# Performance work log

Measured on AMD Instinct MI355X. Metric: run time of the kernel, lower is better.

## Reference

```python
import jax, jax.numpy as jnp
import numpy as np

N, IN_DIM, OUT_DIM, NUM_EXPERTS, TOP_K = 8192, 1024, 1024, 8, 2


def setup_inputs() -> dict:
    key = jax.random.key(0)
    ks = jax.random.split(key, 5)
    s_in = 1.0 / np.sqrt(IN_DIM)
    x = jax.random.normal(ks[0], (N, IN_DIM), dtype=jnp.float32)
    # per-expert Linear weights: [E, in, out] (torch Linear weight is [out,in]; we store transposed)
    W = jax.random.uniform(ks[1], (NUM_EXPERTS, IN_DIM, OUT_DIM), jnp.float32, -s_in, s_in)
    b = jax.random.uniform(ks[2], (NUM_EXPERTS, OUT_DIM), jnp.float32, -s_in, s_in)
    Wg = jax.random.uniform(ks[3], (IN_DIM, NUM_EXPERTS), jnp.float32, -s_in, s_in)
    bg = jax.random.uniform(ks[4], (NUM_EXPERTS,), jnp.float32, -s_in, s_in)
    return {"x": x, "W": W, "b": b, "Wg": Wg, "bg": bg}


def reference(x, W, b, Wg, bg):
    # gating scores [N, E]
    scores = x @ Wg + bg
    # top-k mask
    _, top_idx = jax.lax.top_k(scores, TOP_K)  # [N, k]
    mask = jnp.zeros_like(scores).at[jnp.arange(x.shape[0])[:, None], top_idx].set(1.0)
    masked = jnp.where(mask == 0, -jnp.inf, scores)
    gating_weights = jax.nn.softmax(masked, axis=-1)  # [N, E]
    # all-expert linear: [N, E, out]
    expert_outputs = jnp.einsum('ni,eio->neo', x, W) + b
    # weighted combine over experts
    return jnp.einsum('ne,neo->no', gating_weights, expert_outputs)
```

## Files before the change

kernel.cpp:

```cpp
#include <hip/hip_runtime.h>

#define N_TOK 8192
#define IN_DIM 1024
#define OUT_DIM 1024
#define NE 8
#define TILE_SH 12288

typedef short short8 __attribute__((ext_vector_type(8)));
typedef float f32x4 __attribute__((ext_vector_type(4)));
typedef ushort ushort4v __attribute__((ext_vector_type(4)));

__device__ __forceinline__ ushort f2bf(float f) {
    union { float f; unsigned u; } v; v.f = f;
    unsigned u = v.u;
    unsigned r = (u + 0x7fffu + ((u >> 16) & 1u)) >> 16;
    return (ushort)r;
}

__device__ __forceinline__ float bf2f(short s) {
    union { unsigned u; float f; } v;
    v.u = ((unsigned)(unsigned short)s) << 16;
    return v.f;
}

__device__ __forceinline__ void gl_lds16(const short* g, short* l) {
    __builtin_amdgcn_global_load_lds(
        (const __attribute__((address_space(1))) unsigned int*)g,
        (__attribute__((address_space(3))) unsigned int*)l, 16, 0, 0);
}

__global__ __launch_bounds__(256) void prep(const float* __restrict__ x,
                                            const float* __restrict__ Wg,
                                            const float* __restrict__ bg,
                                            const float* __restrict__ W,
                                            short* __restrict__ xb,
                                            short* __restrict__ wt,
                                            unsigned* __restrict__ choice,
                                            float2* __restrict__ wts) {
    __shared__ ushort tile[32][33];
    int bid = blockIdx.x;
    int t = threadIdx.x;
    if (bid < 512) {
        int wid = t >> 6, lane = t & 63;
        int tok0 = bid * 16 + wid * 4;
        float acc[4][8];
        #pragma unroll
        for (int tk = 0; tk < 4; ++tk)
            #pragma unroll
            for (int e = 0; e < 8; ++e) acc[tk][e] = 0.f;

        #pragma unroll
        for (int it = 0; it < 4; ++it) {
            int j = it * 256 + lane * 4;
            float4 wa[4], wb[4];
            #pragma unroll
            for (int r = 0; r < 4; ++r) {
                wa[r] = *(const float4*)(Wg + (size_t)(j + r) * 8);
                wb[r] = *(const float4*)(Wg + (size_t)(j + r) * 8 + 4);
            }
            #pragma unroll
            for (int tk = 0; tk < 4; ++tk) {
                const float* xr = x + (size_t)(tok0 + tk) * IN_DIM;
                float4 v = *(const float4*)(xr + j);
                ushort4v o;
                o[0] = f2bf(v.x); o[1] = f2bf(v.y); o[2] = f2bf(v.z); o[3] = f2bf(v.w);
                *(ushort4v*)(xb + (size_t)(tok0 + tk) * IN_DIM + j) = o;
                #pragma unroll
                for (int r = 0; r < 4; ++r) {
                    float xv = (r == 0) ? v.x : (r == 1) ? v.y : (r == 2) ? v.z : v.w;
                    acc[tk][0] += xv * wa[r].x; acc[tk][1] += xv * wa[r].y;
                    acc[tk][2] += xv * wa[r].z; acc[tk][3] += xv * wa[r].w;
                    acc[tk][4] += xv * wb[r].x; acc[tk][5] += xv * wb[r].y;
                    acc[tk][6] += xv * wb[r].z; acc[tk][7] += xv * wb[r].w;
                }
            }
        }
        #pragma unroll
        for (int tk = 0; tk < 4; ++tk)
            #pragma unroll
            for (int e = 0; e < 8; ++e)
                #pragma unroll
                for (int off = 32; off; off >>= 1)
                    acc[tk][e] += __shfl_xor(acc[tk][e], off, 64);
        if (lane == 0) {
            #pragma unroll
            for (int tk = 0; tk < 4; ++tk) {
                float s[8];
                #pragma unroll
                for (int e = 0; e < 8; ++e) s[e] = acc[tk][e] + bg[e];
                int i0 = 0;
                #pragma unroll
                for (int e = 1; e < 8; ++e) if (s[e] > s[i0]) i0 = e;
                int i1 = (i0 == 0) ? 1 : 0;
                #pragma unroll
                for (int e = 0; e < 8; ++e) if (e != i0 && s[e] > s[i1]) i1 = e;
                float e0 = 1.f, e1 = __expf(s[i1] - s[i0]);
                float inv = 1.f / (e0 + e1);
                choice[tok0 + tk] = (unsigned)i0 | ((unsigned)i1 << 8);
                wts[tok0 + tk] = make_float2(e0 * inv, e1 * inv);
            }
        }
    } else {
        int id = bid - 512;
        int nt = id & 31, kt = (id >> 5) & 31, e = id >> 10;
        int r = t >> 3;
        int c4 = (t & 7) * 4;
        const float4 v = *(const float4*)(W + (((size_t)e * 1024 + kt * 32 + r) * 1024) + nt * 32 + c4);
        tile[c4 + 0][r] = f2bf(v.x);
        tile[c4 + 1][r] = f2bf(v.y);
        tile[c4 + 2][r] = f2bf(v.z);
        tile[c4 + 3][r] = f2bf(v.w);
        __syncthreads();
        int n = t >> 3, kq = (t & 7) * 4;
        ushort4v o;
        o[0] = tile[n][kq + 0]; o[1] = tile[n][kq + 1];
        o[2] = tile[n][kq + 2]; o[3] = tile[n][kq + 3];
        *(ushort4v*)(wt + (((size_t)e * 1024 + nt * 32 + n) * 1024) + kt * 32 + kq) = o;
    }
}

__global__ __launch_bounds__(1024) void bucket(const unsigned* __restrict__ choice,
                                               int* __restrict__ counts,
                                               int* __restrict__ entries,
                                               int* __restrict__ inv0,
                                               int* __restrict__ inv1) {
    int e = blockIdx.x;
    int t = threadIdx.x;
    int wid = t >> 6, lane = t & 63;
    __shared__ int wsum[16];
    unsigned c[8];
    #pragma unroll
    for (int chunk = 0; chunk < 8; ++chunk) c[chunk] = choice[chunk * 1024 + t];
    int base = 0;
    #pragma unroll
    for (int chunk = 0; chunk < 8; ++chunk) {
        int tok = chunk * 1024 + t;
        int which = ((int)(c[chunk] & 255u) == e) ? 0
                  : (((int)((c[chunk] >> 8) & 255u) == e) ? 1 : -1);
        unsigned long long m = __ballot(which >= 0);
        if (lane == 0) wsum[wid] = __popcll(m);
        __syncthreads();
        int woff = base;
        #pragma unroll
        for (int i = 0; i < 16; ++i) if (i < wid) woff += wsum[i];
        int tot = 0;
        #pragma unroll
        for (int i = 0; i < 16; ++i) tot += wsum[i];
        if (which >= 0) {
            int rank = __popcll(m & ((1ull << lane) - 1ull));
            int idx = woff + rank;
            entries[e * N_TOK + idx] = tok;
            if (which == 0) inv0[tok] = idx; else inv1[tok] = idx;
        }
        base += tot;
        __syncthreads();
    }
    if (t == 0) counts[e] = base;
}

__global__ __launch_bounds__(256, 2) void moe_gemm(const short* __restrict__ xb,
                                                   const short* __restrict__ wt,
                                                   const float* __restrict__ bias,
                                                   const int* __restrict__ counts,
                                                   const int* __restrict__ entries,
                                                   short* __restrict__ ys) {
    int lin = blockIdx.x;
    int e = lin & 7;
    int inner = lin >> 3;
    int ct = inner & 3, rt = inner >> 2;
    int cnt = counts[e];
    if (rt * 128 >= cnt) return;
    int rows = min(128, cnt - rt * 128);
    int base_e = 0;
    #pragma unroll
    for (int i = 0; i < NE; ++i) base_e += (i < e) ? counts[i] : 0;

    __shared__ __align__(16) short lds[3 * TILE_SH];
    __shared__ int tok_sh[128];

    int t = threadIdx.x, wid = t >> 6, lane = t & 63;
    int ebase = e * N_TOK + rt * 128;
    if (t < 128) tok_sh[t] = (t < rows) ? entries[ebase + t] : entries[ebase];
    __syncthreads();

    int chunkoff = (((t & 3) ^ ((t >> 2) & 3)) * 8);
    const short* asrc0 = xb + (size_t)tok_sh[t >> 2] * IN_DIM + chunkoff;
    const short* asrc1 = xb + (size_t)tok_sh[64 + (t >> 2)] * IN_DIM + chunkoff;
    const short* bsrc0 = wt + ((size_t)e * OUT_DIM + ct * 256 + (t >> 2)) * IN_DIM + chunkoff;
    const short* bsrc1 = bsrc0 + (size_t)64 * IN_DIM;
    const short* bsrc2 = bsrc0 + (size_t)128 * IN_DIM;
    const short* bsrc3 = bsrc0 + (size_t)192 * IN_DIM;
    int dst8 = t * 8;

    int wr = wid >> 1, wc = wid & 1;
    int frow = lane & 15, fslot = lane >> 4;
    int rslot = (fslot ^ (frow & 3)) * 8;
    int aoff[4], boff[8];
    #pragma unroll
    for (int mi = 0; mi < 4; ++mi) aoff[mi] = (wr * 64 + mi * 16 + frow) * 32 + rslot;
    #pragma unroll
    for (int ni = 0; ni < 8; ++ni) boff[ni] = (wc * 128 + ni * 16 + frow) * 32 + rslot;

    f32x4 acc[4][8];
    #pragma unroll
    for (int mi = 0; mi < 4; ++mi)
        #pragma unroll
        for (int ni = 0; ni < 8; ++ni) acc[mi][ni] = (f32x4)(0.0f);

    short8 caf[4], cbf[8];

#define STAGE(BUF, KT)                                                        \
    {                                                                         \
        short* nb = lds + (BUF) * TILE_SH;                                    \
        int nk = (KT) * 32;                                                   \
        gl_lds16(asrc0 + nk, nb + dst8);                                      \
        gl_lds16(asrc1 + nk, nb + 2048 + dst8);                               \
        gl_lds16(bsrc0 + nk, nb + 4096 + dst8);                               \
        gl_lds16(bsrc1 + nk, nb + 6144 + dst8);                               \
        gl_lds16(bsrc2 + nk, nb + 8192 + dst8);                               \
        gl_lds16(bsrc3 + nk, nb + 10240 + dst8);                              \
    }

#define LOADFRAGS(BUF)                                                        \
    {                                                                         \
        const short* Ab = lds + (BUF) * TILE_SH;                              \
        const short* Bb = Ab + 4096;                                          \
        _Pragma("unroll")                                                     \
        for (int mi = 0; mi < 4; ++mi) caf[mi] = *(const short8*)(Ab + aoff[mi]); \
        _Pragma("unroll")                                                     \
        for (int ni = 0; ni < 8; ++ni) cbf[ni] = *(const short8*)(Bb + boff[ni]); \
    }

#define GITER(NXTBUF, STGBUF, KTN, VN, DO_STAGE, DO_TAIL)                     \
    {                                                                         \
        if (DO_STAGE) STAGE(STGBUF, KTN);                                     \
        _Pragma("unroll")                                                     \
        for (int mi = 0; mi < 4; ++mi)                                        \
            _Pragma("unroll")                                                 \
            for (int ni = 0; ni < 8; ++ni)                                    \
                acc[mi][ni] = __builtin_amdgcn_mfma_f32_16x16x32_bf16(        \
                    caf[mi], cbf[ni], acc[mi][ni], 0, 0, 0);                  \
        asm volatile("s_waitcnt vmcnt(" VN ")" ::: "memory");                 \
        __builtin_amdgcn_s_barrier();                                         \
        __builtin_amdgcn_sched_barrier(0);   \
        if (DO_TAIL) LOADFRAGS(NXTBUF);                                       \
    }

    STAGE(0, 0);
    STAGE(1, 1);
    asm volatile("s_waitcnt vmcnt(6)" ::: "memory");
    __builtin_amdgcn_s_barrier();
    __builtin_amdgcn_sched_barrier(0);
    LOADFRAGS(0);

    for (int kt = 0; kt < 30; kt += 3) {
        GITER(1, 2, kt + 2, "6", 1, 1);
        GITER(2, 0, kt + 3, "6", 1, 1);
        GITER(0, 1, kt + 4, "6", 1, 1);
    }
    GITER(1, 0, 0, "0", 0, 1);
    GITER(0, 0, 0, "0", 0, 0);

#undef GITER
#undef LOADFRAGS
#undef STAGE

    __syncthreads();
    short* ep = lds;
    const float* be = bias + (size_t)e * OUT_DIM;
    #pragma unroll
    for (int ni = 0; ni < 8; ++ni) {
        int col = wc * 128 + ni * 16 + frow;
        float bv = be[ct * 256 + col];
        #pragma unroll
        for (int mi = 0; mi < 4; ++mi) {
            int rb_ = wr * 64 + mi * 16 + fslot * 4;
            #pragma unroll
            for (int r = 0; r < 4; ++r)
                ep[(rb_ + r) * 268 + col] = (short)f2bf(acc[mi][ni][r] + bv);
        }
    }
    __syncthreads();
    #pragma unroll
    for (int k = 0; k < 16; ++k) {
        int f = t + k * 256;
        int row = f >> 5, cw = f & 31;
        if (row < rows) {
            short8 v = *(const short8*)(ep + row * 268 + cw * 8);
            *(short8*)(ys + ((size_t)(base_e + rt * 128 + row)) * OUT_DIM
                       + ct * 256 + cw * 8) = v;
        }
    }
}

__global__ __launch_bounds__(256) void combine(const short* __restrict__ ys,
                                               const unsigned* __restrict__ choice,
                                               const float2* __restrict__ wts,
                                               const int* __restrict__ inv0,
                                               const int* __restrict__ inv1,
                                               const int* __restrict__ counts,
                                               float* __restrict__ out) {
    __shared__ int bases[8];
    if (threadIdx.x < 8) {
        int s = 0;
        #pragma unroll
        for (int i = 0; i < 8; ++i) s += (i < (int)threadIdx.x) ? counts[i] : 0;
        bases[threadIdx.x] = s;
    }
    __syncthreads();
    int tok = blockIdx.x * 2 + (threadIdx.x >> 7);
    int c8 = (threadIdx.x & 127) * 8;
    unsigned ch = choice[tok];
    float2 w = wts[tok];
    int p0 = bases[ch & 255u] + inv0[tok];
    int p1 = bases[(ch >> 8) & 255u] + inv1[tok];
    short8 a = *(const short8*)(ys + (size_t)p0 * OUT_DIM + c8);
    short8 b = *(const short8*)(ys + (size_t)p1 * OUT_DIM + c8);
    float* op = out + (size_t)tok * OUT_DIM + c8;
    float4 o0, o1;
    o0.x = w.x * bf2f(a[0]) + w.y * bf2f(b[0]);
    o0.y = w.x * bf2f(a[1]) + w.y * bf2f(b[1]);
    o0.z = w.x * bf2f(a[2]) + w.y * bf2f(b[2]);
    o0.w = w.x * bf2f(a[3]) + w.y * bf2f(b[3]);
    o1.x = w.x * bf2f(a[4]) + w.y * bf2f(b[4]);
    o1.y = w.x * bf2f(a[5]) + w.y * bf2f(b[5]);
    o1.z = w.x * bf2f(a[6]) + w.y * bf2f(b[6]);
    o1.w = w.x * bf2f(a[7]) + w.y * bf2f(b[7]);
    *(float4*)op = o0;
    *(float4*)(op + 4) = o1;
}

extern "C" void kernel_launch(void* const* d_in, const int* in_sizes, int n_in,
                              void* d_out, int out_size, void* d_ws, size_t ws_size,
                              hipStream_t stream) {
    const float* x  = (const float*)d_in[0];
    const float* W  = (const float*)d_in[1];
    const float* b  = (const float*)d_in[2];
    const float* Wg = (const float*)d_in[3];
    const float* bg = (const float*)d_in[4];
    float* out = (float*)d_out;

    char* ws = (char*)d_ws;
    short* xb        = (short*)(ws);
    short* wt        = (short*)(ws + 16777216);
    unsigned* choice = (unsigned*)(ws + 33554432);
    float2* wts      = (float2*)(ws + 33587200);
    int* inv0        = (int*)(ws + 33652736);
    int* inv1        = (int*)(ws + 33685504);
    int* entries     = (int*)(ws + 33718272);
    int* counts      = (int*)(ws + 34242560);
    short* ys        = (short*)(ws + 34242624);

    prep<<<8704, 256, 0, stream>>>(x, Wg, bg, W, xb, wt, choice, wts);
    bucket<<<8, 1024, 0, stream>>>(choice, counts, entries, inv0, inv1);
    moe_gemm<<<2048, 256, 0, stream>>>(xb, wt, b, counts, entries, ys);
    combine<<<4096, 256, 0, stream>>>(ys, choice, wts, inv0, inv1, counts, out);
}
```

Baseline: 102.3 us.

## Pre-swizzle expert weights into MFMA fragment layout and load B directly to registers

The prep kernel now writes bf16 expert weights in a fragment-major layout, so each lane's 8-element B operand for a 16x16x32 MFMA is contiguous. The GEMM then loads B fragments straight from global memory into double-buffered registers instead of staging them through LDS. Only A (gathered token rows) goes through LDS, into per-wave private double buffers, which removes the block-wide barriers from the K loop. In exchange, B tiles shared by waves are no longer reused through LDS, so each wave fetches its own B from global memory or L2, and register pressure grows from the two B fragment sets.

```diff
diff --git a/kernel.cpp b/kernel.cpp
--- a/kernel.cpp
+++ b/kernel.cpp
@@ -4,7 +4,6 @@
 #define IN_DIM 1024
 #define OUT_DIM 1024
 #define NE 8
-#define TILE_SH 12288
 
 typedef short short8 __attribute__((ext_vector_type(8)));
 typedef float f32x4 __attribute__((ext_vector_type(4)));
@@ -34,7 +33,7 @@
                                             const float* __restrict__ bg,
                                             const float* __restrict__ W,
                                             short* __restrict__ xb,
-                                            short* __restrict__ wt,
+                                            short* __restrict__ wtf,
                                             unsigned* __restrict__ choice,
                                             float2* __restrict__ wts) {
     __shared__ ushort tile[32][33];
@@ -111,11 +110,15 @@
         tile[c4 + 2][r] = f2bf(v.z);
         tile[c4 + 3][r] = f2bf(v.w);
         __syncthreads();
-        int n = t >> 3, kq = (t & 7) * 4;
+        int n = nt * 32 + (t >> 3);
+        int kq = (t & 7) * 4;
+        int nb = n >> 4, fr = n & 15;
+        int ks = kq >> 3, kr = kq & 7;
         ushort4v o;
-        o[0] = tile[n][kq + 0]; o[1] = tile[n][kq + 1];
-        o[2] = tile[n][kq + 2]; o[3] = tile[n][kq + 3];
-        *(ushort4v*)(wt + (((size_t)e * 1024 + nt * 32 + n) * 1024) + kt * 32 + kq) = o;
+        o[0] = tile[t >> 3][kq + 0]; o[1] = tile[t >> 3][kq + 1];
+        o[2] = tile[t >> 3][kq + 2]; o[3] = tile[t >> 3][kq + 3];
+        *(ushort4v*)(wtf + (((size_t)e * 64 + nb) * 32 + kt) * 512
+                     + ks * 128 + fr * 8 + kr) = o;
     }
 }
 
@@ -159,7 +162,7 @@
 }
 
 __global__ __launch_bounds__(256, 2) void moe_gemm(const short* __restrict__ xb,
-                                                   const short* __restrict__ wt,
+                                                   const short* __restrict__ wtf,
                                                    const float* __restrict__ bias,
                                                    const int* __restrict__ counts,
                                                    const int* __restrict__ entries,
@@ -175,7 +178,7 @@
     #pragma unroll
     for (int i = 0; i < NE; ++i) base_e += (i < e) ? counts[i] : 0;
 
-    __shared__ __align__(16) short lds[3 * TILE_SH];
+    __shared__ __align__(16) short lds[34304];
     __shared__ int tok_sh[128];
 
     int t = threadIdx.x, wid = t >> 6, lane = t & 63;
@@ -183,23 +186,23 @@
     if (t < 128) tok_sh[t] = (t < rows) ? entries[ebase + t] : entries[ebase];
     __syncthreads();
 
-    int chunkoff = (((t & 3) ^ ((t >> 2) & 3)) * 8);
-    const short* asrc0 = xb + (size_t)tok_sh[t >> 2] * IN_DIM + chunkoff;
-    const short* asrc1 = xb + (size_t)tok_sh[64 + (t >> 2)] * IN_DIM + chunkoff;
-    const short* bsrc0 = wt + ((size_t)e * OUT_DIM + ct * 256 + (t >> 2)) * IN_DIM + chunkoff;
-    const short* bsrc1 = bsrc0 + (size_t)64 * IN_DIM;
-    const short* bsrc2 = bsrc0 + (size_t)128 * IN_DIM;
-    const short* bsrc3 = bsrc0 + (size_t)192 * IN_DIM;
-    int dst8 = t * 8;
-
     int wr = wid >> 1, wc = wid & 1;
     int frow = lane & 15, fslot = lane >> 4;
-    int rslot = (fslot ^ (frow & 3)) * 8;
-    int aoff[4], boff[8];
-    #pragma unroll
-    for (int mi = 0; mi < 4; ++mi) aoff[mi] = (wr * 64 + mi * 16 + frow) * 32 + rslot;
-    #pragma unroll
-    for (int ni = 0; ni < 8; ++ni) boff[ni] = (wc * 128 + ni * 16 + frow) * 32 + rslot;
+
+    int chunkoff = (((lane & 3) ^ ((lane >> 2) & 3)) * 8);
+    const short* asrc[4];
+    #pragma unroll
+    for (int i = 0; i < 4; ++i)
+        asrc[i] = xb + (size_t)tok_sh[wr * 64 + i * 16 + (lane >> 2)] * IN_DIM + chunkoff;
+    short* apriv = lds + wid * 4096;
+    int adst = lane * 8;
+
+    int rslot = ((fslot ^ (frow & 3)) * 8);
+    int aoff[4];
+    #pragma unroll
+    for (int mi = 0; mi < 4; ++mi) aoff[mi] = (mi * 16 + frow) * 32 + rslot;
+
+    const short* bbase = wtf + ((size_t)e * 64 + ct * 16 + wc * 8) * 32 * 512 + lane * 8;
 
     f32x4 acc[4][8];
     #pragma unroll
@@ -207,63 +210,54 @@
         #pragma unroll
         for (int ni = 0; ni < 8; ++ni) acc[mi][ni] = (f32x4)(0.0f);
 
-    short8 caf[4], cbf[8];
-
-#define STAGE(BUF, KT)                                                        \
+    short8 caf[4], cbfE[8], cbfO[8];
+
+#define STAGEA(PAR, KT)                                                       \
     {                                                                         \
-        short* nb = lds + (BUF) * TILE_SH;                                    \
+        short* ab = apriv + (PAR) * 2048;                                     \
         int nk = (KT) * 32;                                                   \
-        gl_lds16(asrc0 + nk, nb + dst8);                                      \
-        gl_lds16(asrc1 + nk, nb + 2048 + dst8);                               \
-        gl_lds16(bsrc0 + nk, nb + 4096 + dst8);                               \
-        gl_lds16(bsrc1 + nk, nb + 6144 + dst8);                               \
-        gl_lds16(bsrc2 + nk, nb + 8192 + dst8);                               \
-        gl_lds16(bsrc3 + nk, nb + 10240 + dst8);                              \
-    }
-
-#define LOADFRAGS(BUF)                                                        \
+        gl_lds16(asrc[0] + nk, ab + adst);                                    \
+        gl_lds16(asrc[1] + nk, ab + 512 + adst);                              \
+        gl_lds16(asrc[2] + nk, ab + 1024 + adst);                             \
+        gl_lds16(asrc[3] + nk, ab + 1536 + adst);                             \
+    }
+
+#define LOADB(KT, CBF)                                                        \
     {                                                                         \
-        const short* Ab = lds + (BUF) * TILE_SH;                              \
-        const short* Bb = Ab + 4096;                                          \
+        const short* bp = bbase + (size_t)(KT) * 512;                         \
         _Pragma("unroll")                                                     \
-        for (int mi = 0; mi < 4; ++mi) caf[mi] = *(const short8*)(Ab + aoff[mi]); \
+        for (int ni = 0; ni < 8; ++ni)                                        \
+            CBF[ni] = *(const short8*)(bp + (size_t)ni * 16384);              \
+    }
+
+#define AITER(PAR, KTN, CBFC, CBFN, DO_NEXT, VN)                              \
+    {                                                                         \
+        if (DO_NEXT) { STAGEA((PAR) ^ 1, KTN); LOADB(KTN, CBFN); }            \
+        asm volatile("s_waitcnt vmcnt(" VN ")" ::: "memory");                 \
+        const short* ab = apriv + (PAR) * 2048;                               \
         _Pragma("unroll")                                                     \
-        for (int ni = 0; ni < 8; ++ni) cbf[ni] = *(const short8*)(Bb + boff[ni]); \
-    }
-
-#define GITER(NXTBUF, STGBUF, KTN, VN, DO_STAGE, DO_TAIL)                     \
-    {                                                                         \
-        if (DO_STAGE) STAGE(STGBUF, KTN);                                     \
+        for (int mi = 0; mi < 4; ++mi) caf[mi] = *(const short8*)(ab + aoff[mi]); \
         _Pragma("unroll")                                                     \
         for (int mi = 0; mi < 4; ++mi)                                        \
             _Pragma("unroll")                                                 \
             for (int ni = 0; ni < 8; ++ni)                                    \
                 acc[mi][ni] = __builtin_amdgcn_mfma_f32_16x16x32_bf16(        \
-                    caf[mi], cbf[ni], acc[mi][ni], 0, 0, 0);                  \
-        asm volatile("s_waitcnt vmcnt(" VN ")" ::: "memory");                 \
-        __builtin_amdgcn_s_barrier();                                         \
-        __builtin_amdgcn_sched_barrier(0);   \
-        if (DO_TAIL) LOADFRAGS(NXTBUF);                                       \
-    }
-
-    STAGE(0, 0);
-    STAGE(1, 1);
-    asm volatile("s_waitcnt vmcnt(6)" ::: "memory");
-    __builtin_amdgcn_s_barrier();
-    __builtin_amdgcn_sched_barrier(0);
-    LOADFRAGS(0);
-
-    for (int kt = 0; kt < 30; kt += 3) {
-        GITER(1, 2, kt + 2, "6", 1, 1);
-        GITER(2, 0, kt + 3, "6", 1, 1);
-        GITER(0, 1, kt + 4, "6", 1, 1);
-    }
-    GITER(1, 0, 0, "0", 0, 1);
-    GITER(0, 0, 0, "0", 0, 0);
-
-#undef GITER
-#undef LOADFRAGS
-#undef STAGE
+                    caf[mi], CBFC[ni], acc[mi][ni], 0, 0, 0);                 \
+    }
+
+    STAGEA(0, 0);
+    LOADB(0, cbfE);
+
+    for (int p = 0; p < 15; ++p) {
+        AITER(0, 2 * p + 1, cbfE, cbfO, 1, "12");
+        AITER(1, 2 * p + 2, cbfO, cbfE, 1, "12");
+    }
+    AITER(0, 31, cbfE, cbfO, 1, "12");
+    AITER(1, 0, cbfO, cbfE, 0, "0");
+
+#undef AITER
+#undef LOADB
+#undef STAGEA
 
     __syncthreads();
     short* ep = lds;
@@ -342,7 +336,7 @@
 
     char* ws = (char*)d_ws;
     short* xb        = (short*)(ws);
-    short* wt        = (short*)(ws + 16777216);
+    short* wtf       = (short*)(ws + 16777216);
     unsigned* choice = (unsigned*)(ws + 33554432);
     float2* wts      = (float2*)(ws + 33587200);
     int* inv0        = (int*)(ws + 33652736);
@@ -351,8 +345,8 @@
     int* counts      = (int*)(ws + 34242560);
     short* ys        = (short*)(ws + 34242624);
 
-    prep<<<8704, 256, 0, stream>>>(x, Wg, bg, W, xb, wt, choice, wts);
+    prep<<<8704, 256, 0, stream>>>(x, Wg, bg, W, xb, wtf, choice, wts);
     bucket<<<8, 1024, 0, stream>>>(choice, counts, entries, inv0, inv1);
-    moe_gemm<<<2048, 256, 0, stream>>>(xb, wt, b, counts, entries, ys);
+    moe_gemm<<<2048, 256, 0, stream>>>(xb, wtf, b, counts, entries, ys);
     combine<<<4096, 256, 0, stream>>>(ys, choice, wts, inv0, inv1, counts, out);
 }
```

Result: no change. 103.3 us (+1.0%).

## Switch MoE GEMM to 512-thread blocks with 32x32x16 MFMA tiles

Applied to the files above, without the earlier changes.

Moves the expert GEMM from 4 waves doing 16x16x32 MFMAs over 64x128 wave tiles to 8 waves doing 32x32x16 MFMAs over 64x64 wave tiles. The LDS staging layout becomes chunk-major without XOR swizzling, so each lane reads contiguous 16-byte fragments, and each stage issues fewer global-to-LDS loads per thread. The aim is higher MFMA efficiency and more waves to hide latency. The cost is more threads per block competing for LDS capacity, and the epilogue scatter is rewritten for the 32x32 accumulator layout.

```diff
diff --git a/kernel.cpp b/kernel.cpp
--- a/kernel.cpp
+++ b/kernel.cpp
@@ -7,7 +7,7 @@
 #define TILE_SH 12288
 
 typedef short short8 __attribute__((ext_vector_type(8)));
-typedef float f32x4 __attribute__((ext_vector_type(4)));
+typedef float f32x16 __attribute__((ext_vector_type(16)));
 typedef ushort ushort4v __attribute__((ext_vector_type(4)));
 
 __device__ __forceinline__ ushort f2bf(float f) {
@@ -158,7 +158,7 @@
     if (t == 0) counts[e] = base;
 }
 
-__global__ __launch_bounds__(256, 2) void moe_gemm(const short* __restrict__ xb,
+__global__ __launch_bounds__(512, 4) void moe_gemm(const short* __restrict__ xb,
                                                    const short* __restrict__ wt,
                                                    const float* __restrict__ bias,
                                                    const int* __restrict__ counts,
@@ -183,80 +183,87 @@
     if (t < 128) tok_sh[t] = (t < rows) ? entries[ebase + t] : entries[ebase];
     __syncthreads();
 
-    int chunkoff = (((t & 3) ^ ((t >> 2) & 3)) * 8);
-    const short* asrc0 = xb + (size_t)tok_sh[t >> 2] * IN_DIM + chunkoff;
-    const short* asrc1 = xb + (size_t)tok_sh[64 + (t >> 2)] * IN_DIM + chunkoff;
-    const short* bsrc0 = wt + ((size_t)e * OUT_DIM + ct * 256 + (t >> 2)) * IN_DIM + chunkoff;
-    const short* bsrc1 = bsrc0 + (size_t)64 * IN_DIM;
-    const short* bsrc2 = bsrc0 + (size_t)128 * IN_DIM;
-    const short* bsrc3 = bsrc0 + (size_t)192 * IN_DIM;
+    int srow = t & 127, schunk = t >> 7;
+    const short* asrc  = xb + (size_t)tok_sh[srow] * IN_DIM + schunk * 8;
+    const short* bsrc0 = wt + ((size_t)e * OUT_DIM + ct * 256 + srow) * IN_DIM + schunk * 8;
+    const short* bsrc1 = bsrc0 + (size_t)128 * IN_DIM;
     int dst8 = t * 8;
 
-    int wr = wid >> 1, wc = wid & 1;
-    int frow = lane & 15, fslot = lane >> 4;
-    int rslot = (fslot ^ (frow & 3)) * 8;
-    int aoff[4], boff[8];
-    #pragma unroll
-    for (int mi = 0; mi < 4; ++mi) aoff[mi] = (wr * 64 + mi * 16 + frow) * 32 + rslot;
-    #pragma unroll
-    for (int ni = 0; ni < 8; ++ni) boff[ni] = (wc * 128 + ni * 16 + frow) * 32 + rslot;
-
-    f32x4 acc[4][8];
-    #pragma unroll
-    for (int mi = 0; mi < 4; ++mi)
-        #pragma unroll
-        for (int ni = 0; ni < 8; ++ni) acc[mi][ni] = (f32x4)(0.0f);
-
-    short8 caf[4], cbf[8];
+    int wr = wid >> 2, wc = wid & 3;
+    int l31 = lane & 31, lhi = lane >> 5;
+    int aoff[2][2], boff[2][2];
+    #pragma unroll
+    for (int ks = 0; ks < 2; ++ks) {
+        int chunk = ks * 2 + lhi;
+        #pragma unroll
+        for (int mi = 0; mi < 2; ++mi)
+            aoff[ks][mi] = chunk * 1024 + (wr * 64 + mi * 32 + l31) * 8;
+        #pragma unroll
+        for (int ni = 0; ni < 2; ++ni) {
+            int rowg = wc * 64 + ni * 32 + l31;
+            boff[ks][ni] = 4096 + (rowg >> 7) * 4096 + chunk * 1024 + (rowg & 127) * 8;
+        }
+    }
+
+    f32x16 acc[2][2];
+    #pragma unroll
+    for (int mi = 0; mi < 2; ++mi)
+        #pragma unroll
+        for (int ni = 0; ni < 2; ++ni) acc[mi][ni] = (f32x16)(0.0f);
+
+    short8 caf[2][2], cbf[2][2];
 
 #define STAGE(BUF, KT)                                                        \
     {                                                                         \
         short* nb = lds + (BUF) * TILE_SH;                                    \
         int nk = (KT) * 32;                                                   \
-        gl_lds16(asrc0 + nk, nb + dst8);                                      \
-        gl_lds16(asrc1 + nk, nb + 2048 + dst8);                               \
+        gl_lds16(asrc + nk, nb + dst8);                                       \
         gl_lds16(bsrc0 + nk, nb + 4096 + dst8);                               \
-        gl_lds16(bsrc1 + nk, nb + 6144 + dst8);                               \
-        gl_lds16(bsrc2 + nk, nb + 8192 + dst8);                               \
-        gl_lds16(bsrc3 + nk, nb + 10240 + dst8);                              \
+        gl_lds16(bsrc1 + nk, nb + 8192 + dst8);                               \
     }
 
 #define LOADFRAGS(BUF)                                                        \
     {                                                                         \
         const short* Ab = lds + (BUF) * TILE_SH;                              \
-        const short* Bb = Ab + 4096;                                          \
         _Pragma("unroll")                                                     \
-        for (int mi = 0; mi < 4; ++mi) caf[mi] = *(const short8*)(Ab + aoff[mi]); \
-        _Pragma("unroll")                                                     \
-        for (int ni = 0; ni < 8; ++ni) cbf[ni] = *(const short8*)(Bb + boff[ni]); \
+        for (int ks = 0; ks < 2; ++ks) {                                      \
+            _Pragma("unroll")                                                 \
+            for (int mi = 0; mi < 2; ++mi)                                    \
+                caf[ks][mi] = *(const short8*)(Ab + aoff[ks][mi]);            \
+            _Pragma("unroll")                                                 \
+            for (int ni = 0; ni < 2; ++ni)                                    \
+                cbf[ks][ni] = *(const short8*)(Ab + boff[ks][ni]);            \
+        }                                                                     \
     }
 
 #define GITER(NXTBUF, STGBUF, KTN, VN, DO_STAGE, DO_TAIL)                     \
     {                                                                         \
         if (DO_STAGE) STAGE(STGBUF, KTN);                                     \
         _Pragma("unroll")                                                     \
-        for (int mi = 0; mi < 4; ++mi)                                        \
+        for (int ks = 0; ks < 2; ++ks)                                        \
             _Pragma("unroll")                                                 \
-            for (int ni = 0; ni < 8; ++ni)                                    \
-                acc[mi][ni] = __builtin_amdgcn_mfma_f32_16x16x32_bf16(        \
-                    caf[mi], cbf[ni], acc[mi][ni], 0, 0, 0);                  \
+            for (int mi = 0; mi < 2; ++mi)                                    \
+                _Pragma("unroll")                                             \
+                for (int ni = 0; ni < 2; ++ni)                                \
+                    acc[mi][ni] = __builtin_amdgcn_mfma_f32_32x32x16_bf16(    \
+                        caf[ks][mi], cbf[ks][ni], acc[mi][ni], 0, 0, 0);      \
         asm volatile("s_waitcnt vmcnt(" VN ")" ::: "memory");                 \
         __builtin_amdgcn_s_barrier();                                         \
-        __builtin_amdgcn_sched_barrier(0);   \
+        __builtin_amdgcn_sched_barrier(0);                                    \
         if (DO_TAIL) LOADFRAGS(NXTBUF);                                       \
     }
 
     STAGE(0, 0);
     STAGE(1, 1);
-    asm volatile("s_waitcnt vmcnt(6)" ::: "memory");
+    asm volatile("s_waitcnt vmcnt(3)" ::: "memory");
     __builtin_amdgcn_s_barrier();
     __builtin_amdgcn_sched_barrier(0);
     LOADFRAGS(0);
 
     for (int kt = 0; kt < 30; kt += 3) {
-        GITER(1, 2, kt + 2, "6", 1, 1);
-        GITER(2, 0, kt + 3, "6", 1, 1);
-        GITER(0, 1, kt + 4, "6", 1, 1);
+        GITER(1, 2, kt + 2, "3", 1, 1);
+        GITER(2, 0, kt + 3, "3", 1, 1);
+        GITER(0, 1, kt + 4, "3", 1, 1);
     }
     GITER(1, 0, 0, "0", 0, 1);
     GITER(0, 0, 0, "0", 0, 0);
@@ -267,26 +274,29 @@
 
     __syncthreads();
     short* ep = lds;
-    const float* be = bias + (size_t)e * OUT_DIM;
-    #pragma unroll
-    for (int ni = 0; ni < 8; ++ni) {
-        int col = wc * 128 + ni * 16 + frow;
-        float bv = be[ct * 256 + col];
-        #pragma unroll
-        for (int mi = 0; mi < 4; ++mi) {
-            int rb_ = wr * 64 + mi * 16 + fslot * 4;
-            #pragma unroll
-            for (int r = 0; r < 4; ++r)
-                ep[(rb_ + r) * 268 + col] = (short)f2bf(acc[mi][ni][r] + bv);
+    const float* be = bias + (size_t)e * OUT_DIM + ct * 256;
+    #pragma unroll
+    for (int ni = 0; ni < 2; ++ni) {
+        int col = wc * 64 + ni * 32 + l31;
+        float bv = be[col];
+        #pragma unroll
+        for (int mi = 0; mi < 2; ++mi) {
+            f32x16 a = acc[mi][ni];
+            int rbase = wr * 64 + mi * 32 + 4 * lhi;
+            #pragma unroll
+            for (int reg = 0; reg < 16; ++reg) {
+                int row = rbase + (reg & 3) + 8 * (reg >> 2);
+                ep[row * 264 + col] = (short)f2bf(a[reg] + bv);
+            }
         }
     }
     __syncthreads();
     #pragma unroll
-    for (int k = 0; k < 16; ++k) {
-        int f = t + k * 256;
+    for (int k = 0; k < 8; ++k) {
+        int f = t + k * 512;
         int row = f >> 5, cw = f & 31;
         if (row < rows) {
-            short8 v = *(const short8*)(ep + row * 268 + cw * 8);
+            short8 v = *(const short8*)(ep + row * 264 + cw * 8);
             *(short8*)(ys + ((size_t)(base_e + rt * 128 + row)) * OUT_DIM
                        + ct * 256 + cw * 8) = v;
         }
@@ -353,6 +363,6 @@
 
     prep<<<8704, 256, 0, stream>>>(x, Wg, bg, W, xb, wt, choice, wts);
     bucket<<<8, 1024, 0, stream>>>(choice, counts, entries, inv0, inv1);
-    moe_gemm<<<2048, 256, 0, stream>>>(xb, wt, b, counts, entries, ys);
+    moe_gemm<<<2048, 512, 0, stream>>>(xb, wt, b, counts, entries, ys);
     combine<<<4096, 256, 0, stream>>>(ys, choice, wts, inv0, inv1, counts, out);
 }
```

New measurement: 135.6 us. +32.5%, slower.
